# Performance work log

Hardware: AMD Instinct MI355X
Metric: run time of the kernel (lower is better)

The kernel has to match this reference:

```python
import jax, jax.numpy as jnp
import numpy as np

EMBED_DIM = 768
NUM_HEADS = 12
HEAD_DIM = EMBED_DIM // NUM_HEADS
SCALE = HEAD_DIM ** -0.5
LN_EPS = 1e-5


def layer_norm(x, gamma, beta):
    mu = jnp.mean(x, axis=-1, keepdims=True)
    var = jnp.var(x, axis=-1, keepdims=True)
    return (x - mu) * jax.lax.rsqrt(var + LN_EPS) * gamma + beta


def setup_inputs() -> dict:
    key = jax.random.key(0)
    ks = jax.random.split(key, 10)
    B, N, M, C = 4, 4096, 256, EMBED_DIM
    inp = {
        "input_tokens": jax.random.normal(ks[0], (B, N, C), dtype=jnp.float32),
        "query_tokens": jax.random.normal(ks[1], (B, M, C), dtype=jnp.float32),
        "Wq": jax.random.normal(ks[2], (C, C), dtype=jnp.float32) * 0.02,
        "bq": jnp.zeros((C,), dtype=jnp.float32),
        "Wk": jax.random.normal(ks[3], (C, C), dtype=jnp.float32) * 0.02,
        "bk": jnp.zeros((C,), dtype=jnp.float32),
        "Wv": jax.random.normal(ks[4], (C, C), dtype=jnp.float32) * 0.02,
        "bv": jnp.zeros((C,), dtype=jnp.float32),
        "gq_ln": jnp.ones((C,), dtype=jnp.float32),
        "bq_ln": jnp.zeros((C,), dtype=jnp.float32),
        "gk_ln": jnp.ones((C,), dtype=jnp.float32),
        "bk_ln": jnp.zeros((C,), dtype=jnp.float32),
    }
    return inp


def reference(input_tokens, query_tokens, Wq, bq, Wk, bk, Wv, bv,
              gq_ln, bq_ln, gk_ln, bk_ln):
    B, N, C = input_tokens.shape
    _, M, _ = query_tokens.shape
    H, D = NUM_HEADS, HEAD_DIM

    # v: Linear only (no LayerNorm on the attn=None path)
    v = (input_tokens @ Wv.T + bv).reshape(B, N, H, D).transpose(0, 2, 1, 3)   # [B,H,N,D]
    # q, k: Linear -> LayerNorm over full embed_dim, then split heads
    q = layer_norm(query_tokens @ Wq.T + bq, gq_ln, bq_ln)
    q = q.reshape(B, M, H, D).transpose(0, 2, 1, 3) * SCALE                    # [B,H,M,D]
    k = layer_norm(input_tokens @ Wk.T + bk, gk_ln, bk_ln)
    k = k.reshape(B, N, H, D).transpose(0, 2, 1, 3)                            # [B,H,N,D]

    attn = jax.nn.softmax(jnp.einsum('bhmd,bhnd->bhmn', q, k), axis=-1)        # [B,H,M,N]
    out = jnp.einsum('bhmn,bhnd->bhmd', attn, v)                               # [B,H,M,D]
    out = out.transpose(0, 2, 1, 3).reshape(B, M, C)
    return (query_tokens + out, attn)
```

## Files before the change

kernel.cpp:

```cpp
#include <hip/hip_runtime.h>
#include <math.h>

#define BB 4
#define NN 4096
#define MM 256
#define CC 768
#define HH 12
#define DD 64
#define SCALEF 0.125f
#define LN_EPSF 1e-5f

typedef __attribute__((ext_vector_type(4))) float f32x4;
typedef __attribute__((ext_vector_type(16))) float f32x16;
typedef __attribute__((ext_vector_type(8))) _Float16 f16x8;
typedef __attribute__((ext_vector_type(4))) _Float16 f16x4;

__device__ __forceinline__ void gldh(const _Float16* g, _Float16* l) {
    __builtin_amdgcn_global_load_lds(
        (const __attribute__((address_space(1))) void*)g,
        (__attribute__((address_space(3))) void*)l, 16, 0, 0);
}

__global__ __launch_bounds__(256) void conv_all(
    const float* __restrict__ x0, _Float16* __restrict__ y0, long long n0,
    const float* __restrict__ x1, _Float16* __restrict__ y1, long long n1,
    const float* __restrict__ x2, _Float16* __restrict__ y2, long long n2,
    const float* __restrict__ x3, _Float16* __restrict__ y3, long long n3,
    const float* __restrict__ x4, _Float16* __restrict__ y4, long long n4)
{
    long long i = ((long long)blockIdx.x * 256 + threadIdx.x) * 8;
    const long long total = n0 + n1 + n2 + n3 + n4;
    const long long stride = (long long)gridDim.x * 256 * 8;
    for (; i < total; i += stride) {
        const float* x; _Float16* y; long long off = i;
        if (off < n0) { x = x0; y = y0; }
        else if ((off -= n0) < n1) { x = x1; y = y1; }
        else if ((off -= n1) < n2) { x = x2; y = y2; }
        else if ((off -= n2) < n3) { x = x3; y = y3; }
        else { off -= n3; x = x4; y = y4; }
        float4 a = *(const float4*)(x + off);
        float4 b = *(const float4*)(x + off + 4);
        f16x8 o;
        o[0] = (_Float16)a.x; o[1] = (_Float16)a.y;
        o[2] = (_Float16)a.z; o[3] = (_Float16)a.w;
        o[4] = (_Float16)b.x; o[5] = (_Float16)b.y;
        o[6] = (_Float16)b.z; o[7] = (_Float16)b.w;
        *(f16x8*)(y + off) = o;
    }
}

__global__ __launch_bounds__(256) void proj_kv_f16(
    const _Float16* __restrict__ Xh,
    const _Float16* __restrict__ X2h,
    const _Float16* __restrict__ Wkh, const _Float16* __restrict__ Wqh,
    const _Float16* __restrict__ Wvh,
    const float* __restrict__ bk, const float* __restrict__ bq,
    const float* __restrict__ bv,
    _Float16* __restrict__ Klin, _Float16* __restrict__ Qlin,
    _Float16* __restrict__ Vth)
{
    __shared__ _Float16 As[3][4096];
    __shared__ _Float16 Bks[3][4096];
    __shared__ _Float16 Bvs[3][4096];

    const int bid = blockIdx.x;
    const _Float16* Ag; const _Float16* Bkg;
    const float* biask; _Float16* outk;
    bool hasV;
    int bm, bn;
    if (bid < 768) {
        bm = bid & 127; bn = bid >> 7;
        Ag = Xh; Bkg = Wkh; biask = bk; outk = Klin; hasV = true;
    } else {
        const int sid = bid - 768;
        bm = sid & 7; bn = sid >> 3;
        Ag = X2h; Bkg = Wqh; biask = bq; outk = Qlin; hasV = false;
    }
    const int row0 = bm * 128, col0 = bn * 128;

    const int tid = threadIdx.x;
    const int w = tid >> 6, lane = tid & 63;
    const int wr = w >> 1, wc = w & 1;
    const int fr = lane & 15, kg = lane >> 4;

    f32x4 acck[4][4], accv[4][4];
#pragma unroll
    for (int m = 0; m < 4; ++m)
#pragma unroll
        for (int n = 0; n < 4; ++n) {
            acck[m][n] = (f32x4){0.f, 0.f, 0.f, 0.f};
            accv[m][n] = (f32x4){0.f, 0.f, 0.f, 0.f};
        }

#define STAGE(sel, kt)                                                           \
    do {                                                                         \
        const int kk = (kt) << 5;                                                \
        _Pragma("unroll")                                                        \
        for (int i = 0; i < 2; ++i) {                                            \
            const int cbase = (i * 4 + w) * 64;                                  \
            const int c = cbase + lane;                                          \
            const int row = c >> 2, ks = (c & 3) << 3;                           \
            gldh(Ag  + (size_t)(row0 + row) * CC + kk + ks, &As[sel][cbase * 8]);\
            gldh(Bkg + (size_t)(col0 + row) * CC + kk + ks, &Bks[sel][cbase * 8]);\
            gldh(Wvh + (size_t)(col0 + row) * CC + kk + ks, &Bvs[sel][cbase * 8]);\
        }                                                                        \
    } while (0)

    STAGE(0, 0);
    STAGE(1, 1);
    const int nk = CC >> 5;
    for (int kt = 0; kt < nk; ++kt) {
        if (kt + 1 < nk) asm volatile("s_waitcnt vmcnt(6)" ::: "memory");
        else             asm volatile("s_waitcnt vmcnt(0)" ::: "memory");
        __builtin_amdgcn_s_barrier();
        __builtin_amdgcn_sched_barrier(0);
        if (kt + 2 < nk) STAGE((kt + 2) % 3, kt + 2);
        const int cur = kt % 3;
        const _Float16* lA = As[cur];
        const _Float16* lBk = Bks[cur];
        const _Float16* lBv = Bvs[cur];
        f16x8 a[4];
#pragma unroll
        for (int m = 0; m < 4; ++m)
            a[m] = *(const f16x8*)(lA + (wr * 64 + m * 16 + fr) * 32 + kg * 8);
#pragma unroll
        for (int n = 0; n < 4; ++n) {
            f16x8 bkf = *(const f16x8*)(lBk + (wc * 64 + n * 16 + fr) * 32 + kg * 8);
            __builtin_amdgcn_s_setprio(1);
#pragma unroll
            for (int m = 0; m < 4; ++m)
                acck[m][n] = __builtin_amdgcn_mfma_f32_16x16x32_f16(
                    a[m], bkf, acck[m][n], 0, 0, 0);
            __builtin_amdgcn_s_setprio(0);
            f16x8 bvf = *(const f16x8*)(lBv + (wc * 64 + n * 16 + fr) * 32 + kg * 8);
            __builtin_amdgcn_s_setprio(1);
#pragma unroll
            for (int m = 0; m < 4; ++m)
                accv[m][n] = __builtin_amdgcn_mfma_f32_16x16x32_f16(
                    a[m], bvf, accv[m][n], 0, 0, 0);
            __builtin_amdgcn_s_setprio(0);
        }
    }
#undef STAGE

    {
        float bvv[4];
#pragma unroll
        for (int n = 0; n < 4; ++n)
            bvv[n] = biask[col0 + wc * 64 + n * 16 + fr];
#pragma unroll
        for (int m = 0; m < 4; ++m)
#pragma unroll
            for (int n = 0; n < 4; ++n) {
                const int col = col0 + wc * 64 + n * 16 + fr;
#pragma unroll
                for (int r = 0; r < 4; ++r) {
                    const int row = row0 + wr * 64 + m * 16 + kg * 4 + r;
                    outk[(size_t)row * CC + col] = (_Float16)(acck[m][n][r] + bvv[n]);
                }
            }
    }
    if (hasV) {
        const int b = row0 >> 12;
        const int rb = row0 & 4095;
#pragma unroll
        for (int n = 0; n < 4; ++n) {
            const int cg = col0 + wc * 64 + n * 16 + fr;
            const int hh = cg >> 6, d = cg & 63;
            const float bb = bv[cg];
            _Float16* vrow = Vth + ((size_t)((b * HH + hh) * DD + d)) * NN + rb + wr * 64;
#pragma unroll
            for (int m = 0; m < 4; ++m) {
                f16x4 v4;
#pragma unroll
                for (int r = 0; r < 4; ++r)
                    v4[r] = (_Float16)(accv[m][n][r] + bb);
                *(f16x4*)(vrow + m * 16 + kg * 4) = v4;
            }
        }
    }
}

__global__ __launch_bounds__(256) void ln_rows_f16(
    const _Float16* __restrict__ Klin, const _Float16* __restrict__ Qlin,
    _Float16* __restrict__ Kh, _Float16* __restrict__ Qh,
    const float* __restrict__ gk, const float* __restrict__ bkln,
    const float* __restrict__ gq, const float* __restrict__ bqln)
{
    int row = blockIdx.x;
    const _Float16* y; _Float16* o;
    const float* g; const float* be; float scale;
    if (row < BB * NN) {
        y = Klin + (size_t)row * CC; o = Kh + (size_t)row * CC;
        g = gk; be = bkln; scale = 1.0f;
    } else {
        row -= BB * NN;
        y = Qlin + (size_t)row * CC; o = Qh + (size_t)row * CC;
        g = gq; be = bqln; scale = SCALEF;
    }
    const int tid = threadIdx.x;
    float x0 = (float)y[tid], x1 = (float)y[tid + 256], x2 = (float)y[tid + 512];
    float s = x0 + x1 + x2;
    float q = x0 * x0 + x1 * x1 + x2 * x2;
#pragma unroll
    for (int o2 = 32; o2 >= 1; o2 >>= 1) {
        s += __shfl_xor(s, o2, 64);
        q += __shfl_xor(q, o2, 64);
    }
    __shared__ float sh_s[4], sh_q[4];
    const int w = tid >> 6;
    if ((tid & 63) == 0) { sh_s[w] = s; sh_q[w] = q; }
    __syncthreads();
    s = sh_s[0] + sh_s[1] + sh_s[2] + sh_s[3];
    q = sh_q[0] + sh_q[1] + sh_q[2] + sh_q[3];
    const float mu  = s * (1.f / 768.f);
    const float var = q * (1.f / 768.f) - mu * mu;
    const float inv = rsqrtf(var + LN_EPSF);
    o[tid]       = (_Float16)(((x0 - mu) * inv * g[tid]       + be[tid])       * scale);
    o[tid + 256] = (_Float16)(((x1 - mu) * inv * g[tid + 256] + be[tid + 256]) * scale);
    o[tid + 512] = (_Float16)(((x2 - mu) * inv * g[tid + 512] + be[tid + 512]) * scale);
}

__global__ __launch_bounds__(256, 4) void attn_stats(
    const _Float16* __restrict__ Qh,
    const _Float16* __restrict__ Kh,
    float* __restrict__ stats)
{
    __shared__ __align__(16) unsigned char smem[37888];
    _Float16* Kl = (_Float16*)smem;
    _Float16* Ql = (_Float16*)(smem + 32768);
    float (*red)[32][2] = (float(*)[32][2])(smem + 36864);

    const int tid = threadIdx.x;
    const int w = tid >> 6, lane = tid & 63;
    const int l5 = lane >> 5, lm = lane & 31;
    const int bid = blockIdx.x;
    const int mt = bid / 192;
    const int rem = bid % 192;
    const int bh = rem >> 2, ns = rem & 3;
    const int h = bh % HH, b = bh / HH;
    const int qr0 = mt * 32;
    const int nb = ns * 1024;

#define STAGEK(sel, c0)                                                         \
    _Pragma("unroll")                                                           \
    for (int i = 0; i < 4; ++i) {                                               \
        const int L = i * 256 + tid;                                            \
        const int n = L >> 3, pos = L & 7;                                      \
        gldh(Kh + (size_t)(b * NN + (c0) + n) * CC + h * DD + ((pos ^ (n & 7)) << 3), \
             &Kl[(sel) * 8192 + (i * 256 + w * 64) * 8]);                       \
    }

    {
        const int n = tid >> 3, pos = tid & 7;
        gldh(Qh + (size_t)(b * MM + qr0 + n) * CC + h * DD + ((pos ^ (n & 7)) << 3),
             &Ql[(w * 64) * 8]);
    }
    STAGEK(0, nb);
    __syncthreads();
    f16x8 qf[4];
#pragma unroll
    for (int ks = 0; ks < 4; ++ks)
        qf[ks] = *(const f16x8*)&Ql[lm * 64 + (((ks * 2 + l5) ^ (lm & 7)) << 3)];

    const int nl = w * 32 + lm;

    float mrun = -1e30f, srun = 0.f;
    int cur = 0;
    for (int c = 0; c < 8; ++c) {
        if (c) __syncthreads();
        if (c + 1 < 8) STAGEK(cur ^ 1, nb + (c + 1) * 128);
        const _Float16* Kb = Kl + cur * 8192;
        f32x16 s;
#pragma unroll
        for (int r = 0; r < 16; ++r) s[r] = 0.f;
        __builtin_amdgcn_s_setprio(1);
#pragma unroll
        for (int ks = 0; ks < 4; ++ks) {
            f16x8 kf = *(const f16x8*)&Kb[nl * 64 + (((ks * 2 + l5) ^ (nl & 7)) << 3)];
            s = __builtin_amdgcn_mfma_f32_32x32x16_f16(kf, qf[ks], s, 0, 0, 0);
        }
        __builtin_amdgcn_s_setprio(0);
        float cmax = s[0];
#pragma unroll
        for (int r = 1; r < 16; ++r) cmax = fmaxf(cmax, s[r]);
        cmax = fmaxf(cmax, __shfl_xor(cmax, 32, 64));
        const float nm = fmaxf(mrun, cmax);
        float cs = 0.f;
#pragma unroll
        for (int r = 0; r < 16; ++r) cs += __expf(s[r] - nm);
        cs += __shfl_xor(cs, 32, 64);
        srun = srun * __expf(mrun - nm) + cs;
        mrun = nm;
        cur ^= 1;
    }
    if (lane < 32) { red[w][lane][0] = mrun; red[w][lane][1] = srun; }
    __syncthreads();
    if (w == 0 && lane < 32) {
        float M = -1e30f;
#pragma unroll
        for (int ww = 0; ww < 4; ++ww) M = fmaxf(M, red[ww][lane][0]);
        float S = 0.f;
#pragma unroll
        for (int ww = 0; ww < 4; ++ww) S += red[ww][lane][1] * __expf(red[ww][lane][0] - M);
        float* sp = stats + ((size_t)((bh * 8 + mt) * 32 + lane)) * 8 + ns * 2;
        sp[0] = M; sp[1] = S;
    }
#undef STAGEK
}

__global__ __launch_bounds__(256, 2) void attn_main(
    const _Float16* __restrict__ Qh, const _Float16* __restrict__ Kh,
    const _Float16* __restrict__ Vt,
    const float* __restrict__ stats, const float* __restrict__ qtok,
    float* __restrict__ attn, float* __restrict__ out0)
{
    __shared__ __align__(16) unsigned char smem[77824];
    _Float16* Kl = (_Float16*)smem;
    _Float16* Vl = (_Float16*)(smem + 32768);
    _Float16* Ql = (_Float16*)(smem + 65536);
    _Float16* Pl = (_Float16*)(smem + 69632);
    float* rbuf = (float*)smem;

    const int tid = threadIdx.x;
    const int w = tid >> 6, lane = tid & 63;
    const int l5 = lane >> 5, lm = lane & 31;
    const int bh = blockIdx.x % 48;
    const int mt = blockIdx.x / 48;
    const int h = bh % HH, b = bh / HH;
    const int qr0 = mt * 32;

#define STAGEK(sel, c0)                                                         \
    _Pragma("unroll")                                                           \
    for (int i = 0; i < 4; ++i) {                                               \
        const int L = i * 256 + tid;                                            \
        const int n = L >> 3, pos = L & 7;                                      \
        gldh(Kh + (size_t)(b * NN + (c0) + n) * CC + h * DD + ((pos ^ (n & 7)) << 3), \
             &Kl[(sel) * 8192 + (i * 256 + w * 64) * 8]);                       \
    }
#define STAGEV(sel, c0)                                                         \
    _Pragma("unroll")                                                           \
    for (int i = 0; i < 4; ++i) {                                               \
        const int L = i * 256 + tid;                                            \
        const int d = L >> 4, pos = L & 15;                                     \
        const int blk = (pos & 8) | ((pos & 7) ^ (d & 7));                      \
        gldh(Vt + (size_t)(bh * DD + d) * NN + (c0) + blk * 8,                  \
             &Vl[(sel) * 8192 + (i * 256 + w * 64) * 8]);                       \
    }

    float M, invS;
    {
        const float* sp = stats + ((size_t)((bh * 8 + mt) * 32 + lm)) * 8;
        M = -1e30f;
#pragma unroll
        for (int n2 = 0; n2 < 4; ++n2) M = fmaxf(M, sp[n2 * 2]);
        float S = 0.f;
#pragma unroll
        for (int n2 = 0; n2 < 4; ++n2) S += sp[n2 * 2 + 1] * __expf(sp[n2 * 2] - M);
        invS = 1.f / S;
    }

    {
        const int n = tid >> 3, pos = tid & 7;
        gldh(Qh + (size_t)(b * MM + qr0 + n) * CC + h * DD + ((pos ^ (n & 7)) << 3),
             &Ql[(w * 64) * 8]);
    }
    STAGEK(0, 0); STAGEV(0, 0);
    __syncthreads();
    f16x8 qf[4];
#pragma unroll
    for (int ks = 0; ks < 4; ++ks)
        qf[ks] = *(const f16x8*)&Ql[lm * 64 + (((ks * 2 + l5) ^ (lm & 7)) << 3)];

    const int nl = w * 32 + lm;

    f32x16 oacc[2];
#pragma unroll
    for (int dt = 0; dt < 2; ++dt)
#pragma unroll
        for (int r = 0; r < 16; ++r) oacc[dt][r] = 0.f;

    int cur = 0;
    for (int c = 0; c < 32; ++c) {
        if (c) {
            asm volatile("s_waitcnt vmcnt(4)" ::: "memory");
            __builtin_amdgcn_s_barrier();
            __builtin_amdgcn_sched_barrier(0);
        }
        if (c + 1 < 32) { STAGEK(cur ^ 1, (c + 1) * 128); STAGEV(cur ^ 1, (c + 1) * 128); }
        __builtin_amdgcn_sched_barrier(0);
        const _Float16* Kb = Kl + cur * 8192;
        const _Float16* Vb = Vl + cur * 8192;
        f32x16 s;
#pragma unroll
        for (int r = 0; r < 16; ++r) s[r] = 0.f;
        __builtin_amdgcn_s_setprio(1);
#pragma unroll
        for (int ks = 0; ks < 4; ++ks) {
            f16x8 kf = *(const f16x8*)&Kb[nl * 64 + (((ks * 2 + l5) ^ (nl & 7)) << 3)];
            s = __builtin_amdgcn_mfma_f32_32x32x16_f16(kf, qf[ks], s, 0, 0, 0);
        }
        __builtin_amdgcn_s_setprio(0);
#pragma unroll
        for (int q = 0; q < 4; ++q) {
            f16x4 ph;
#pragma unroll
            for (int r = 0; r < 4; ++r)
                ph[r] = (_Float16)(__expf(s[q * 4 + r] - M) * invS);
            const int blk16 = w * 4 + q;
            const int pos = (blk16 & 8) | ((blk16 & 7) ^ (lm & 7));
            *(f16x4*)&Pl[lm * 128 + pos * 8 + l5 * 4] = ph;
        }
        __builtin_amdgcn_s_setprio(1);
#pragma unroll
        for (int ks = 0; ks < 2; ++ks) {
            const int blk16 = w * 4 + ks * 2 + l5;
            const int posP = (blk16 & 8) | ((blk16 & 7) ^ (lm & 7));
            f16x8 pf = *(const f16x8*)&Pl[lm * 128 + posP * 8];
#pragma unroll
            for (int dt = 0; dt < 2; ++dt) {
                const int d = dt * 32 + lm;
                const int posV = (blk16 & 8) | ((blk16 & 7) ^ (d & 7));
                f16x8 vf = *(const f16x8*)&Vb[d * 128 + posV * 8];
                oacc[dt] = __builtin_amdgcn_mfma_f32_32x32x16_f16(pf, vf, oacc[dt], 0, 0, 0);
            }
        }
        __builtin_amdgcn_s_setprio(0);
#pragma unroll
        for (int p = 0; p < 4; ++p) {
            const int pr = p >> 1, nh = p & 1;
            const int row = pr * 16 + (lane >> 2);
            const int k = lane & 3;
            const int nn = nh * 16 + k * 4;
            const int j = w * 4 + (nn >> 3);
            const int swz = (j & 8) | ((j & 7) ^ (row & 7));
            f16x4 pv4 = *(const f16x4*)&Pl[row * 128 + swz * 8 + (nn & 7)];
            f32x4 o4;
            o4[0] = (float)pv4[0]; o4[1] = (float)pv4[1];
            o4[2] = (float)pv4[2]; o4[3] = (float)pv4[3];
            __builtin_nontemporal_store(o4,
                (f32x4*)(attn + ((size_t)(bh * MM + qr0 + row)) * NN
                         + c * 128 + w * 32 + nn));
        }
        cur ^= 1;
    }

    __syncthreads();
#pragma unroll
    for (int dt = 0; dt < 2; ++dt)
#pragma unroll
        for (int r = 0; r < 16; ++r) {
            const int mrow = (r & 3) + 8 * (r >> 2) + 4 * l5;
            rbuf[w * 2048 + mrow * 64 + dt * 32 + lm] = oacc[dt][r];
        }
    __syncthreads();
    {
        const int m = tid >> 3, d0 = (tid & 7) * 8;
        const size_t obase = (size_t)(b * MM + qr0 + m) * CC + h * DD + d0;
        f32x4 v0, v1;
#pragma unroll
        for (int j = 0; j < 4; ++j) {
            const int idx = m * 64 + d0 + j;
            v0[j] = rbuf[idx] + rbuf[2048 + idx] + rbuf[4096 + idx] + rbuf[6144 + idx];
        }
#pragma unroll
        for (int j = 0; j < 4; ++j) {
            const int idx = m * 64 + d0 + 4 + j;
            v1[j] = rbuf[idx] + rbuf[2048 + idx] + rbuf[4096 + idx] + rbuf[6144 + idx];
        }
        float4 q0 = *(const float4*)(qtok + obase);
        float4 q1 = *(const float4*)(qtok + obase + 4);
        v0[0] += q0.x; v0[1] += q0.y; v0[2] += q0.z; v0[3] += q0.w;
        v1[0] += q1.x; v1[1] += q1.y; v1[2] += q1.z; v1[3] += q1.w;
        *(f32x4*)(out0 + obase) = v0;
        *(f32x4*)(out0 + obase + 4) = v1;
    }
#undef STAGEK
#undef STAGEV
}

extern "C" void kernel_launch(void* const* d_in, const int* in_sizes, int n_in,
                              void* d_out, int out_size, void* d_ws, size_t ws_size,
                              hipStream_t stream) {
    (void)in_sizes; (void)n_in; (void)out_size; (void)ws_size;
    const float* input_tokens = (const float*)d_in[0];
    const float* query_tokens = (const float*)d_in[1];
    const float* Wq   = (const float*)d_in[2];
    const float* bq   = (const float*)d_in[3];
    const float* Wk   = (const float*)d_in[4];
    const float* bk   = (const float*)d_in[5];
    const float* Wv   = (const float*)d_in[6];
    const float* bv   = (const float*)d_in[7];
    const float* gq   = (const float*)d_in[8];
    const float* bqln = (const float*)d_in[9];
    const float* gk   = (const float*)d_in[10];
    const float* bkln = (const float*)d_in[11];

    float* out0 = (float*)d_out;
    float* attn = out0 + (size_t)BB * MM * CC;

    _Float16* hptr = (_Float16*)d_ws;
    _Float16* Klin = hptr;
    _Float16* Qlin = Klin + (size_t)BB * NN * CC;
    _Float16* Xh   = Qlin + (size_t)BB * MM * CC;
    _Float16* X2h  = Xh   + (size_t)BB * NN * CC;
    _Float16* Wkh  = X2h  + (size_t)BB * MM * CC;
    _Float16* Wqh  = Wkh  + (size_t)CC * CC;
    _Float16* Wvh  = Wqh  + (size_t)CC * CC;
    _Float16* Kh   = Wvh  + (size_t)CC * CC;
    _Float16* Qh   = Kh   + (size_t)BB * NN * CC;
    _Float16* Vt   = Qh   + (size_t)BB * MM * CC;
    float* stats   = (float*)(Vt + (size_t)BB * HH * DD * NN);

    conv_all<<<2048, 256, 0, stream>>>(
        input_tokens, Xh, (long long)BB * NN * CC,
        query_tokens, X2h, (long long)BB * MM * CC,
        Wk, Wkh, (long long)CC * CC,
        Wq, Wqh, (long long)CC * CC,
        Wv, Wvh, (long long)CC * CC);

    proj_kv_f16<<<816, 256, 0, stream>>>(Xh, X2h, Wkh, Wqh, Wvh,
                                         bk, bq, bv, Klin, Qlin, Vt);

    ln_rows_f16<<<BB * NN + BB * MM, 256, 0, stream>>>(Klin, Qlin, Kh, Qh,
                                                       gk, bkln, gq, bqln);

    attn_stats<<<1536, 256, 0, stream>>>(Qh, Kh, stats);
    attn_main<<<384, 256, 0, stream>>>(Qh, Kh, Vt, stats, query_tokens, attn, out0);
}
```

Before: 186.5 us.

## Fuse fp32-to-fp16 activation conversion into projection GEMM A-tile loading

Removes the separate conversion pass over input and query tokens. The projection kernel now loads fp32 activations into registers, converts them to fp16 and writes them to LDS itself, while the weights are still converted by a smaller kernel. The LDS pipeline drops from triple buffering with async global-to-LDS loads to double buffering with __syncthreads, and the A tile now goes through registers. This saves a full fp32 read plus fp16 write and re-read of the large activation tensor, but risks less latency hiding and more register pressure inside the GEMM loop.

```diff
diff --git a/kernel.cpp b/kernel.cpp
--- a/kernel.cpp
+++ b/kernel.cpp
@@ -21,23 +21,19 @@
         (__attribute__((address_space(3))) void*)l, 16, 0, 0);
 }
 
-__global__ __launch_bounds__(256) void conv_all(
-    const float* __restrict__ x0, _Float16* __restrict__ y0, long long n0,
-    const float* __restrict__ x1, _Float16* __restrict__ y1, long long n1,
-    const float* __restrict__ x2, _Float16* __restrict__ y2, long long n2,
-    const float* __restrict__ x3, _Float16* __restrict__ y3, long long n3,
-    const float* __restrict__ x4, _Float16* __restrict__ y4, long long n4)
+__global__ __launch_bounds__(256) void conv_w(
+    const float* __restrict__ x0, _Float16* __restrict__ y0,
+    const float* __restrict__ x1, _Float16* __restrict__ y1,
+    const float* __restrict__ x2, _Float16* __restrict__ y2)
 {
+    const long long seg = (long long)CC * CC;
     long long i = ((long long)blockIdx.x * 256 + threadIdx.x) * 8;
-    const long long total = n0 + n1 + n2 + n3 + n4;
     const long long stride = (long long)gridDim.x * 256 * 8;
-    for (; i < total; i += stride) {
+    for (; i < 3 * seg; i += stride) {
         const float* x; _Float16* y; long long off = i;
-        if (off < n0) { x = x0; y = y0; }
-        else if ((off -= n0) < n1) { x = x1; y = y1; }
-        else if ((off -= n1) < n2) { x = x2; y = y2; }
-        else if ((off -= n2) < n3) { x = x3; y = y3; }
-        else { off -= n3; x = x4; y = y4; }
+        if (off < seg) { x = x0; y = y0; }
+        else if ((off -= seg) < seg) { x = x1; y = y1; }
+        else { off -= seg; x = x2; y = y2; }
         float4 a = *(const float4*)(x + off);
         float4 b = *(const float4*)(x + off + 4);
         f16x8 o;
@@ -50,8 +46,8 @@
 }
 
 __global__ __launch_bounds__(256) void proj_kv_f16(
-    const _Float16* __restrict__ Xh,
-    const _Float16* __restrict__ X2h,
+    const float* __restrict__ Xf,
+    const float* __restrict__ X2f,
     const _Float16* __restrict__ Wkh, const _Float16* __restrict__ Wqh,
     const _Float16* __restrict__ Wvh,
     const float* __restrict__ bk, const float* __restrict__ bq,
@@ -59,22 +55,22 @@
     _Float16* __restrict__ Klin, _Float16* __restrict__ Qlin,
     _Float16* __restrict__ Vth)
 {
-    __shared__ _Float16 As[3][4096];
-    __shared__ _Float16 Bks[3][4096];
-    __shared__ _Float16 Bvs[3][4096];
+    __shared__ _Float16 As[2][4096];
+    __shared__ _Float16 Bks[2][4096];
+    __shared__ _Float16 Bvs[2][4096];
 
     const int bid = blockIdx.x;
-    const _Float16* Ag; const _Float16* Bkg;
+    const float* Af; const _Float16* Bkg;
     const float* biask; _Float16* outk;
     bool hasV;
     int bm, bn;
     if (bid < 768) {
         bm = bid & 127; bn = bid >> 7;
-        Ag = Xh; Bkg = Wkh; biask = bk; outk = Klin; hasV = true;
+        Af = Xf; Bkg = Wkh; biask = bk; outk = Klin; hasV = true;
     } else {
         const int sid = bid - 768;
         bm = sid & 7; bn = sid >> 3;
-        Ag = X2h; Bkg = Wqh; biask = bq; outk = Qlin; hasV = false;
+        Af = X2f; Bkg = Wqh; biask = bq; outk = Qlin; hasV = false;
     }
     const int row0 = bm * 128, col0 = bn * 128;
 
@@ -83,6 +79,9 @@
     const int wr = w >> 1, wc = w & 1;
     const int fr = lane & 15, kg = lane >> 4;
 
+    const int arow = tid >> 1, acol = (tid & 1) * 16;
+    const float* abase = Af + (size_t)(row0 + arow) * CC + acol;
+
     f32x4 acck[4][4], accv[4][4];
 #pragma unroll
     for (int m = 0; m < 4; ++m)
@@ -92,7 +91,32 @@
             accv[m][n] = (f32x4){0.f, 0.f, 0.f, 0.f};
         }
 
-#define STAGE(sel, kt)                                                           \
+    float4 a0, a1, a2, a3;
+
+#define LOADA(kt)                                                                \
+    do {                                                                         \
+        const float* s_ = abase + ((kt) << 5);                                   \
+        a0 = *(const float4*)(s_);      a1 = *(const float4*)(s_ + 4);           \
+        a2 = *(const float4*)(s_ + 8);  a3 = *(const float4*)(s_ + 12);          \
+    } while (0)
+
+#define WRITEA(sel)                                                              \
+    do {                                                                         \
+        f16x8 h0_, h1_;                                                          \
+        h0_[0] = (_Float16)a0.x; h0_[1] = (_Float16)a0.y;                        \
+        h0_[2] = (_Float16)a0.z; h0_[3] = (_Float16)a0.w;                        \
+        h0_[4] = (_Float16)a1.x; h0_[5] = (_Float16)a1.y;                        \
+        h0_[6] = (_Float16)a1.z; h0_[7] = (_Float16)a1.w;                        \
+        h1_[0] = (_Float16)a2.x; h1_[1] = (_Float16)a2.y;                        \
+        h1_[2] = (_Float16)a2.z; h1_[3] = (_Float16)a2.w;                        \
+        h1_[4] = (_Float16)a3.x; h1_[5] = (_Float16)a3.y;                        \
+        h1_[6] = (_Float16)a3.z; h1_[7] = (_Float16)a3.w;                        \
+        _Float16* d_ = &As[sel][arow * 32 + acol];                               \
+        *(f16x8*)d_ = h0_;                                                       \
+        *(f16x8*)(d_ + 8) = h1_;                                                 \
+    } while (0)
+
+#define STAGEB(sel, kt)                                                          \
     do {                                                                         \
         const int kk = (kt) << 5;                                                \
         _Pragma("unroll")                                                        \
@@ -100,22 +124,19 @@
             const int cbase = (i * 4 + w) * 64;                                  \
             const int c = cbase + lane;                                          \
             const int row = c >> 2, ks = (c & 3) << 3;                           \
-            gldh(Ag  + (size_t)(row0 + row) * CC + kk + ks, &As[sel][cbase * 8]);\
             gldh(Bkg + (size_t)(col0 + row) * CC + kk + ks, &Bks[sel][cbase * 8]);\
             gldh(Wvh + (size_t)(col0 + row) * CC + kk + ks, &Bvs[sel][cbase * 8]);\
         }                                                                        \
     } while (0)
 
-    STAGE(0, 0);
-    STAGE(1, 1);
+    LOADA(0);
+    STAGEB(0, 0);
+    WRITEA(0);
     const int nk = CC >> 5;
     for (int kt = 0; kt < nk; ++kt) {
-        if (kt + 1 < nk) asm volatile("s_waitcnt vmcnt(6)" ::: "memory");
-        else             asm volatile("s_waitcnt vmcnt(0)" ::: "memory");
-        __builtin_amdgcn_s_barrier();
-        __builtin_amdgcn_sched_barrier(0);
-        if (kt + 2 < nk) STAGE((kt + 2) % 3, kt + 2);
-        const int cur = kt % 3;
+        __syncthreads();
+        const int cur = kt & 1, nxt = cur ^ 1;
+        if (kt + 1 < nk) { LOADA(kt + 1); STAGEB(nxt, kt + 1); }
         const _Float16* lA = As[cur];
         const _Float16* lBk = Bks[cur];
         const _Float16* lBv = Bvs[cur];
@@ -140,8 +161,11 @@
                     a[m], bvf, accv[m][n], 0, 0, 0);
             __builtin_amdgcn_s_setprio(0);
         }
-    }
-#undef STAGE
+        if (kt + 1 < nk) WRITEA(nxt);
+    }
+#undef LOADA
+#undef WRITEA
+#undef STAGEB
 
     {
         float bvv[4];
@@ -502,9 +526,7 @@
     _Float16* hptr = (_Float16*)d_ws;
     _Float16* Klin = hptr;
     _Float16* Qlin = Klin + (size_t)BB * NN * CC;
-    _Float16* Xh   = Qlin + (size_t)BB * MM * CC;
-    _Float16* X2h  = Xh   + (size_t)BB * NN * CC;
-    _Float16* Wkh  = X2h  + (size_t)BB * MM * CC;
+    _Float16* Wkh  = Qlin + (size_t)BB * MM * CC;
     _Float16* Wqh  = Wkh  + (size_t)CC * CC;
     _Float16* Wvh  = Wqh  + (size_t)CC * CC;
     _Float16* Kh   = Wvh  + (size_t)CC * CC;
@@ -512,14 +534,10 @@
     _Float16* Vt   = Qh   + (size_t)BB * MM * CC;
     float* stats   = (float*)(Vt + (size_t)BB * HH * DD * NN);
 
-    conv_all<<<2048, 256, 0, stream>>>(
-        input_tokens, Xh, (long long)BB * NN * CC,
-        query_tokens, X2h, (long long)BB * MM * CC,
-        Wk, Wkh, (long long)CC * CC,
-        Wq, Wqh, (long long)CC * CC,
-        Wv, Wvh, (long long)CC * CC);
-
-    proj_kv_f16<<<816, 256, 0, stream>>>(Xh, X2h, Wkh, Wqh, Wvh,
+    conv_w<<<512, 256, 0, stream>>>(Wk, Wkh, Wq, Wqh, Wv, Wvh);
+
+    proj_kv_f16<<<816, 256, 0, stream>>>(input_tokens, query_tokens,
+                                         Wkh, Wqh, Wvh,
                                          bk, bq, bv, Klin, Qlin, Vt);
 
     ln_rows_f16<<<BB * NN + BB * MM, 256, 0, stream>>>(Klin, Qlin, Kh, Qh,
```

Result: no change. 184.8 us (-0.9%).
